# Kernel tuning notes

Hardware: AMD Instinct MI355X
Metric: run time of the kernel (lower is better)

Reference implementation:

```python
import jax, jax.numpy as jnp
import numpy as np
import math

IMG_H = 360; IMG_W = 640; S = 72; STRIDE = 8
FH = IMG_H // STRIDE  # 45
FW = IMG_W // STRIDE  # 80
C_IN = 64; C_FEAT = 64
B = 16


def _make_anchors():
    # Replicates LaneATTHead._generate_anchors with lateral_n=72, bottom_n=128.
    anchor_ys = np.linspace(1.0, 0.0, S)
    cut_ys = np.linspace(1.0, 0.0, FH)
    left = [72., 60., 49., 39., 30., 22.]
    right = [108., 120., 131., 141., 150., 158.]
    bottom = [165., 150., 141., 131., 120., 108., 100., 90., 80., 72., 60., 49., 39., 30., 15.]

    def side(angles, nb, x=None, y=None):
        if y is not None:
            sx0 = np.linspace(1.0, 0.0, nb); sy0 = np.full(nb, y)
        else:
            sx0 = np.full(nb, x); sy0 = np.linspace(1.0, 0.0, nb)
        na = len(angles)
        sx = np.repeat(sx0, na); sy = np.repeat(sy0, na)  # start index outer, angle inner
        t = np.tile(np.tan(np.array(angles) * math.pi / 180.0), nb)
        def build(ys):
            a = np.zeros((nb * na, 5 + len(ys)), dtype=np.float32)
            a[:, 2] = 1.0 - sy
            a[:, 3] = sx
            a[:, 5:] = (sx[:, None] + (sy[:, None] - ys[None, :]) / t[:, None]) * IMG_W
            return a
        return build(anchor_ys), build(cut_ys)

    la, lc = side(left, 72, x=0.0)
    ra, rc = side(right, 72, x=1.0)
    ba, bc = side(bottom, 128, y=1.0)
    anchors = np.concatenate([la, ba, ra], axis=0)       # (2784, 77)
    anchors_cut = np.concatenate([lc, bc, rc], axis=0)   # (2784, 50)
    return anchors, anchors_cut


def setup_inputs() -> dict:
    key = jax.random.key(0)
    ks = jax.random.split(key, 4)
    anchors, cuts = _make_anchors()
    scale = IMG_W / FW
    xs = np.round(cuts[:, 5:] / scale).astype(np.int64)
    xs = np.ascontiguousarray(xs[:, ::-1])               # flip along fmap-y
    invalid = (xs < 0) | (xs >= FW)
    xs = np.clip(xs, 0, FW - 1)
    feat_dim = C_FEAT * FH  # 2880
    return {
        "x": jax.random.normal(ks[0], (B, C_IN, FH, FW), jnp.float32),
        "conv_w": jax.random.normal(ks[1], (C_FEAT, C_IN), jnp.float32) * math.sqrt(2.0 / C_FEAT),
        "conv_b": jnp.zeros((C_FEAT,), jnp.float32),
        "cls_w": jax.random.normal(ks[2], (feat_dim, 2), jnp.float32) * 0.01,
        "cls_b": jnp.zeros((2,), jnp.float32),
        "reg_w": jax.random.normal(ks[3], (feat_dim, S + 1), jnp.float32) * 0.01,
        "reg_b": jnp.zeros((S + 1,), jnp.float32),
        "anchors": jnp.asarray(anchors),
        "cut_xs": jnp.asarray(xs, jnp.int32),            # (N, FH)
        "invalid_mask": jnp.asarray(invalid),            # (N, FH) bool
    }


def reference(x, conv_w, conv_b, cls_w, cls_b, reg_w, reg_b, anchors, cut_xs, invalid_mask):
    Bn = x.shape[0]
    N = anchors.shape[0]
    # 1x1 conv
    feat = jnp.einsum('bchw,oc->bohw', x, conv_w) + conv_b[None, :, None, None]
    # anchor feature cutting: out[b,c,n,y] = feat[b,c,y,cut_xs[n,y]]
    ys = jnp.arange(FH)
    g = feat[:, :, ys[None, :], cut_xs]                  # (B, C, N, FH)
    g = jnp.where(invalid_mask[None, None], 0.0, g)
    f = g.transpose(0, 2, 1, 3).reshape(Bn, N, C_FEAT * FH)  # (B, N, 2880), C outer then fh
    cls_logits = f @ cls_w + cls_b                       # (B, N, 2)
    reg = f @ reg_w + reg_b                              # (B, N, 73)
    p24 = jnp.broadcast_to(anchors[None, :, 2:4], (Bn, N, 2))
    out = jnp.concatenate([cls_logits, p24, anchors[None, :, 4:] + reg], axis=-1)  # (B, N, 77)
    return out
```

## Files before the change

### kernel.cpp

```cpp
#include <hip/hip_runtime.h>
#include <stdint.h>

#define FH 45
#define FW 80
#define CIN 64
#define CF 64
#define NANCH 2784
#define BB 16
#define JP 80
#define JN 75
#define MROW (FH * FW)
#define SB ((MROW + 1) * JP)
#define ZOFF (MROW * JP)
#define TOTBN (BB * NANCH)

__global__ __launch_bounds__(256) void k1_weights(
    const float* __restrict__ conv_w, const float* __restrict__ conv_b,
    const float* __restrict__ cls_w, const float* __restrict__ reg_w,
    const int* __restrict__ cut_xs, const uint8_t* __restrict__ invalid,
    float* __restrict__ V, float* __restrict__ biasM, int* __restrict__ off) {
    int blk = blockIdx.x;
    int tid = threadIdx.x;
    if (blk >= 90) {
        int idx = (blk - 90) * 256 + tid;
        if (idx < NANCH * FH) {
            int y = idx % FH;
            off[idx] = invalid[idx] ? ZOFF : (y * FW + cut_xs[idx]) * JP;
        }
        return;
    }
    int y = blk >> 1;
    int j0 = (blk & 1) * 40;
    __shared__ float cw[CF * CIN];
    __shared__ float wl[CF * 40];
    __shared__ float cb[CF];
    for (int i = tid; i < CF * CIN; i += 256) cw[i] = conv_w[i];
    if (tid < CF) cb[tid] = conv_b[tid];
    for (int i = tid; i < CF * 40; i += 256) {
        int c = i / 40, jl = i % 40, j = j0 + jl;
        float v = 0.f;
        if (j < 2) v = cls_w[(c * FH + y) * 2 + j];
        else if (j < JN) v = reg_w[(c * FH + y) * 73 + (j - 2)];
        wl[i] = v;
    }
    __syncthreads();
    int ci = tid & 63;
    int jb = tid >> 6;
    float acc[10];
    #pragma unroll
    for (int k = 0; k < 10; ++k) acc[k] = 0.f;
    for (int c = 0; c < CF; ++c) {
        float a = cw[c * CIN + ci];
        #pragma unroll
        for (int k = 0; k < 10; ++k)
            acc[k] = fmaf(a, wl[c * 40 + jb + 4 * k], acc[k]);
    }
    #pragma unroll
    for (int k = 0; k < 10; ++k)
        V[y * (CIN * JP) + ci * JP + j0 + jb + 4 * k] = acc[k];
    if (tid < 40) {
        float s = 0.f;
        for (int c = 0; c < CF; ++c) s += cb[c] * wl[c * 40 + tid];
        biasM[y * JP + j0 + tid] = s;
    }
}

__global__ __launch_bounds__(256) void k2_feat(
    const float* __restrict__ x, const float* __restrict__ V,
    const float* __restrict__ biasM, float* __restrict__ M) {
    int b = blockIdx.x / FH;
    int y = blockIdx.x % FH;
    __shared__ float xl[CIN * FW];
    __shared__ float vl[CIN * JP];
    __shared__ float bl[JP];
    int tid = threadIdx.x;
    for (int t = tid; t < CIN * FW; t += 256) {
        int ci = t / FW, xc = t % FW;
        xl[t] = x[((b * CIN + ci) * FH + y) * FW + xc];
    }
    const float* vsrc = V + y * (CIN * JP);
    for (int t = tid; t < CIN * JP; t += 256) vl[t] = vsrc[t];
    if (tid < JP) bl[tid] = biasM[y * JP + tid];
    if (y == 0 && tid < JP) M[(size_t)b * SB + ZOFF + tid] = 0.f;
    __syncthreads();
    if (tid < 200) {
        int tx = tid % 20;
        int tj = tid / 20;
        int x0 = tx * 4, jg0 = tj * 8;
        float acc[4][8];
        for (int xx = 0; xx < 4; ++xx)
            for (int jj = 0; jj < 8; ++jj)
                acc[xx][jj] = bl[jg0 + jj];
        for (int ci = 0; ci < CIN; ++ci) {
            float4 xv = *reinterpret_cast<const float4*>(&xl[ci * FW + x0]);
            float4 v0 = *reinterpret_cast<const float4*>(&vl[ci * JP + jg0]);
            float4 v1 = *reinterpret_cast<const float4*>(&vl[ci * JP + jg0 + 4]);
            float xa[4] = {xv.x, xv.y, xv.z, xv.w};
            float va[8] = {v0.x, v0.y, v0.z, v0.w, v1.x, v1.y, v1.z, v1.w};
            for (int xx = 0; xx < 4; ++xx)
                for (int jj = 0; jj < 8; ++jj)
                    acc[xx][jj] = fmaf(xa[xx], va[jj], acc[xx][jj]);
        }
        float* mbase = M + (size_t)b * SB + ((size_t)y * FW) * JP;
        for (int xx = 0; xx < 4; ++xx) {
            float* row = mbase + (size_t)(x0 + xx) * JP + jg0;
            *reinterpret_cast<float4*>(row)     = make_float4(acc[xx][0], acc[xx][1], acc[xx][2], acc[xx][3]);
            *reinterpret_cast<float4*>(row + 4) = make_float4(acc[xx][4], acc[xx][5], acc[xx][6], acc[xx][7]);
        }
    }
}

#define BNB 13
__global__ __launch_bounds__(256) void k3_gather(
    const float* __restrict__ M, const float* __restrict__ anchors,
    const float* __restrict__ cls_b, const float* __restrict__ reg_b,
    const int* __restrict__ off, float* __restrict__ out) {
    __shared__ int sidx[BNB * FH];
    int tid = threadIdx.x;
    int bn0 = blockIdx.x * BNB;
    for (int i = tid; i < BNB * FH; i += 256) {
        int bnl = i / FH, y = i % FH;
        int bn = bn0 + bnl;
        sidx[i] = (bn < TOTBN) ? off[(bn % NANCH) * FH + y] : ZOFF;
    }
    __syncthreads();
    if (tid >= BNB * 19) return;
    int lb = tid / 19;
    int jg = tid % 19;
    int bn = bn0 + lb;
    if (bn >= TOTBN) return;
    int b = bn / NANCH;
    int n = bn % NANCH;
    const float* mb = M + (size_t)b * SB + jg * 4;
    const int* si = sidx + lb * FH;
    float4 s = make_float4(0.f, 0.f, 0.f, 0.f);
    #pragma unroll
    for (int y = 0; y < FH; ++y) {
        int o = si[y];
        float4 v = *reinterpret_cast<const float4*>(mb + o);
        s.x += v.x; s.y += v.y; s.z += v.z; s.w += v.w;
    }
    float sa[4] = {s.x, s.y, s.z, s.w};
    float* dst = out + (size_t)bn * 77;
    const float* arow = anchors + (size_t)n * 77;
    int j0 = jg * 4;
    #pragma unroll
    for (int e = 0; e < 4; ++e) {
        int j = j0 + e;
        if (j < 2)       dst[j]     = sa[e] + cls_b[j];
        else if (j < JN) dst[j + 2] = sa[e] + reg_b[j - 2] + arow[j + 2];
    }
    if (jg == 0) { dst[2] = arow[2]; dst[3] = arow[3]; }
}

extern "C" void kernel_launch(void* const* d_in, const int* in_sizes, int n_in,
                              void* d_out, int out_size, void* d_ws, size_t ws_size,
                              hipStream_t stream) {
    const float* x       = (const float*)d_in[0];
    const float* conv_w  = (const float*)d_in[1];
    const float* conv_b  = (const float*)d_in[2];
    const float* cls_w   = (const float*)d_in[3];
    const float* cls_b   = (const float*)d_in[4];
    const float* reg_w   = (const float*)d_in[5];
    const float* reg_b   = (const float*)d_in[6];
    const float* anchors = (const float*)d_in[7];
    const int* cut_xs    = (const int*)d_in[8];
    const uint8_t* invalid = (const uint8_t*)d_in[9];
    float* out = (float*)d_out;

    float* V     = (float*)d_ws;
    float* biasM = V + FH * CIN * JP;
    float* M     = biasM + FH * JP;
    int*   off   = (int*)(M + (size_t)BB * SB);

    int n_off_blocks = (NANCH * FH + 255) / 256;
    k1_weights<<<90 + n_off_blocks, 256, 0, stream>>>(conv_w, conv_b, cls_w, reg_w,
                                                      cut_xs, invalid, V, biasM, off);
    k2_feat<<<BB * FH, 256, 0, stream>>>(x, V, biasM, M);
    int nblk3 = (TOTBN + BNB - 1) / BNB;
    k3_gather<<<nblk3, 256, 0, stream>>>(M, anchors, cls_b, reg_b, off, out);
}
```

Baseline: 151.3 us.

## Store projected feature table in bf16 and remap gather blocks per batch

The intermediate per-pixel projected table M is now written in bf16, packed two values per word, which halves its footprint and the bytes read by the gather kernel. Each gather thread handles 8 outputs using 16-byte loads and unpacks to fp32 for accumulation. Gather blocks now cover 25 anchors of a single batch image, with batches interleaved across block IDs so that each block's M slice stays cache-local. The bf16 rounding of the 45 summed terms adds numerical error against the fp32 reference.

```diff
diff --git a/kernel.cpp b/kernel.cpp
--- a/kernel.cpp
+++ b/kernel.cpp
@@ -1,4 +1,5 @@
 #include <hip/hip_runtime.h>
+#include <hip/hip_bf16.h>
 #include <stdint.h>
 
 #define FH 45
@@ -13,6 +14,14 @@
 #define SB ((MROW + 1) * JP)
 #define ZOFF (MROW * JP)
 #define TOTBN (BB * NANCH)
+#define ANB 25
+#define CPB ((NANCH + ANB - 1) / ANB)
+
+static __device__ __forceinline__ uint32_t pkbf(float a, float b) {
+    uint32_t lo = (uint32_t)__bfloat16_as_ushort(__float2bfloat16(a));
+    uint32_t hi = (uint32_t)__bfloat16_as_ushort(__float2bfloat16(b));
+    return lo | (hi << 16);
+}
 
 __global__ __launch_bounds__(256) void k1_weights(
     const float* __restrict__ conv_w, const float* __restrict__ conv_b,
@@ -67,7 +76,7 @@
 
 __global__ __launch_bounds__(256) void k2_feat(
     const float* __restrict__ x, const float* __restrict__ V,
-    const float* __restrict__ biasM, float* __restrict__ M) {
+    const float* __restrict__ biasM, __hip_bfloat16* __restrict__ M) {
     int b = blockIdx.x / FH;
     int y = blockIdx.x % FH;
     __shared__ float xl[CIN * FW];
@@ -81,7 +90,8 @@
     const float* vsrc = V + y * (CIN * JP);
     for (int t = tid; t < CIN * JP; t += 256) vl[t] = vsrc[t];
     if (tid < JP) bl[tid] = biasM[y * JP + tid];
-    if (y == 0 && tid < JP) M[(size_t)b * SB + ZOFF + tid] = 0.f;
+    __hip_bfloat16* Mb = M + (size_t)b * SB;
+    if (y == 0 && tid < JP) Mb[ZOFF + tid] = __float2bfloat16(0.f);
     __syncthreads();
     if (tid < 200) {
         int tx = tid % 20;
@@ -101,54 +111,64 @@
                 for (int jj = 0; jj < 8; ++jj)
                     acc[xx][jj] = fmaf(xa[xx], va[jj], acc[xx][jj]);
         }
-        float* mbase = M + (size_t)b * SB + ((size_t)y * FW) * JP;
+        __hip_bfloat16* mbase = Mb + ((size_t)y * FW) * JP;
         for (int xx = 0; xx < 4; ++xx) {
-            float* row = mbase + (size_t)(x0 + xx) * JP + jg0;
-            *reinterpret_cast<float4*>(row)     = make_float4(acc[xx][0], acc[xx][1], acc[xx][2], acc[xx][3]);
-            *reinterpret_cast<float4*>(row + 4) = make_float4(acc[xx][4], acc[xx][5], acc[xx][6], acc[xx][7]);
-        }
-    }
-}
-
-#define BNB 13
+            uint32_t* row = (uint32_t*)(mbase + (size_t)(x0 + xx) * JP + jg0);
+            uint4 pk;
+            pk.x = pkbf(acc[xx][0], acc[xx][1]);
+            pk.y = pkbf(acc[xx][2], acc[xx][3]);
+            pk.z = pkbf(acc[xx][4], acc[xx][5]);
+            pk.w = pkbf(acc[xx][6], acc[xx][7]);
+            *reinterpret_cast<uint4*>(row) = pk;
+        }
+    }
+}
+
 __global__ __launch_bounds__(256) void k3_gather(
-    const float* __restrict__ M, const float* __restrict__ anchors,
+    const __hip_bfloat16* __restrict__ M, const float* __restrict__ anchors,
     const float* __restrict__ cls_b, const float* __restrict__ reg_b,
     const int* __restrict__ off, float* __restrict__ out) {
-    __shared__ int sidx[BNB * FH];
+    __shared__ int sidx[ANB * FH];
     int tid = threadIdx.x;
-    int bn0 = blockIdx.x * BNB;
-    for (int i = tid; i < BNB * FH; i += 256) {
-        int bnl = i / FH, y = i % FH;
-        int bn = bn0 + bnl;
-        sidx[i] = (bn < TOTBN) ? off[(bn % NANCH) * FH + y] : ZOFF;
+    int wg = blockIdx.x;
+    int b = (wg % 8) * 2 + ((wg >> 3) & 1);
+    int chunk = wg >> 4;
+    int n0 = chunk * ANB;
+    int nvalid = NANCH - n0; if (nvalid > ANB) nvalid = ANB;
+    for (int i = tid; i < ANB * FH; i += 256) {
+        int nl = i / FH;
+        sidx[i] = (nl < nvalid) ? off[n0 * FH + i] : ZOFF;
     }
     __syncthreads();
-    if (tid >= BNB * 19) return;
-    int lb = tid / 19;
-    int jg = tid % 19;
-    int bn = bn0 + lb;
-    if (bn >= TOTBN) return;
-    int b = bn / NANCH;
-    int n = bn % NANCH;
-    const float* mb = M + (size_t)b * SB + jg * 4;
+    if (tid >= ANB * 10) return;
+    int lb = tid / 10;
+    int jg = tid % 10;
+    if (lb >= nvalid) return;
+    int n = n0 + lb;
+    const __hip_bfloat16* mb = M + (size_t)b * SB + jg * 8;
     const int* si = sidx + lb * FH;
-    float4 s = make_float4(0.f, 0.f, 0.f, 0.f);
+    float s[8];
+    #pragma unroll
+    for (int e = 0; e < 8; ++e) s[e] = 0.f;
     #pragma unroll
     for (int y = 0; y < FH; ++y) {
         int o = si[y];
-        float4 v = *reinterpret_cast<const float4*>(mb + o);
-        s.x += v.x; s.y += v.y; s.z += v.z; s.w += v.w;
-    }
-    float sa[4] = {s.x, s.y, s.z, s.w};
-    float* dst = out + (size_t)bn * 77;
+        uint4 v = *reinterpret_cast<const uint4*>(mb + o);
+        uint32_t u[4] = {v.x, v.y, v.z, v.w};
+        #pragma unroll
+        for (int p = 0; p < 4; ++p) {
+            s[2 * p]     += __uint_as_float(u[p] << 16);
+            s[2 * p + 1] += __uint_as_float(u[p] & 0xFFFF0000u);
+        }
+    }
+    float* dst = out + ((size_t)b * NANCH + n) * 77;
     const float* arow = anchors + (size_t)n * 77;
-    int j0 = jg * 4;
-    #pragma unroll
-    for (int e = 0; e < 4; ++e) {
+    int j0 = jg * 8;
+    #pragma unroll
+    for (int e = 0; e < 8; ++e) {
         int j = j0 + e;
-        if (j < 2)       dst[j]     = sa[e] + cls_b[j];
-        else if (j < JN) dst[j + 2] = sa[e] + reg_b[j - 2] + arow[j + 2];
+        if (j < 2)       dst[j]     = s[e] + cls_b[j];
+        else if (j < JN) dst[j + 2] = s[e] + reg_b[j - 2] + arow[j + 2];
     }
     if (jg == 0) { dst[2] = arow[2]; dst[3] = arow[3]; }
 }
@@ -170,13 +190,12 @@
 
     float* V     = (float*)d_ws;
     float* biasM = V + FH * CIN * JP;
-    float* M     = biasM + FH * JP;
-    int*   off   = (int*)(M + (size_t)BB * SB);
+    __hip_bfloat16* M = (__hip_bfloat16*)(biasM + FH * JP);
+    int*   off   = (int*)((char*)M + (size_t)BB * SB * sizeof(__hip_bfloat16));
 
     int n_off_blocks = (NANCH * FH + 255) / 256;
     k1_weights<<<90 + n_off_blocks, 256, 0, stream>>>(conv_w, conv_b, cls_w, reg_w,
                                                       cut_xs, invalid, V, biasM, off);
     k2_feat<<<BB * FH, 256, 0, stream>>>(x, V, biasM, M);
-    int nblk3 = (TOTBN + BNB - 1) / BNB;
-    k3_gather<<<nblk3, 256, 0, stream>>>(M, anchors, cls_b, reg_b, off, out);
-}
+    k3_gather<<<16 * CPB, 256, 0, stream>>>(M, anchors, cls_b, reg_b, off, out);
+}
```

Result: faster. 141.9 us (-6.2%).
